# Kernel optimization log

Measured on AMD Instinct MI355X. Metric: run time of the kernel, lower is better.

The kernel has to match this reference:

```python
import jax, jax.numpy as jnp
import numpy as np

DIM, B, H, W = 96, 2, 64, 64
D_INNER, D_STATE, DT_RANK, K = 2 * DIM, 16, 6, 4


def _conv2d(x, w, b=None, padding=0, dilation=1, groups=1):
    out = jax.lax.conv_general_dilated(
        x, w, (1, 1), [(padding, padding)] * 2,
        rhs_dilation=(dilation, dilation),
        dimension_numbers=('NCHW', 'OIHW', 'NCHW'),
        feature_group_count=groups)
    return out if b is None else out + b[None, :, None, None]


def _layernorm(x, g, b, eps=1e-5):
    mu = x.mean(-1, keepdims=True)
    xc = x - mu
    var = (xc * xc).mean(-1, keepdims=True)
    return xc * jax.lax.rsqrt(var + eps) * g + b


def _chan_recal(t, w1, w2):
    s = t.mean((2, 3)) + t.max(axis=(2, 3))          # GAP + GMP, (B,C)
    w = jax.nn.sigmoid(jax.nn.relu(s @ w1.T) @ w2.T)
    return t * w[:, :, None, None]


def _selective_scan(u, delta, A, Bm, Cm, D):
    # u, delta: (B,K,d,L); A: (K,d,N); Bm,Cm: (B,K,N,L); D: (K,d)
    Bsz, Kk, d, L = u.shape
    N = A.shape[-1]
    seq = (jnp.moveaxis(delta, -1, 0), jnp.moveaxis(u, -1, 0),
           jnp.moveaxis(Bm, -1, 0), jnp.moveaxis(Cm, -1, 0))
    h0 = jnp.zeros((Bsz, Kk, d, N), u.dtype)

    def step(h, inp):
        dl, ul, bl, cl = inp  # (B,K,d),(B,K,d),(B,K,N),(B,K,N)
        h = jnp.exp(dl[..., None] * A) * h + (dl * ul)[..., None] * bl[:, :, None, :]
        return h, (h * cl[:, :, None, :]).sum(-1)

    _, ys = jax.lax.scan(step, h0, seq)
    return jnp.moveaxis(ys, 0, -1) + D[None, :, :, None] * u  # (B,K,d,L)


def _ss2d(x, in_proj_w, conv_w, conv_b, x_proj_w, dt_w, dt_b,
          A_logs, Ds, out_norm_g, out_norm_b, out_proj_w):
    Bsz, Hh, Ww, C = x.shape
    d = in_proj_w.shape[0] // 2
    xm, z = jnp.split(x @ in_proj_w.T, 2, axis=-1)
    xm = jnp.transpose(xm, (0, 3, 1, 2))  # (B,d,H,W)
    xm = jax.nn.silu(_conv2d(xm, conv_w, conv_b, padding=1, groups=d))
    L = Hh * Ww
    x_hw = xm.reshape(Bsz, d, L)
    x_wh = jnp.transpose(xm, (0, 1, 3, 2)).reshape(Bsz, d, L)
    xs = jnp.stack([x_hw, x_wh, x_hw[..., ::-1], x_wh[..., ::-1]], axis=1)  # (B,4,d,L)
    x_dbl = jnp.einsum('bkdl,kcd->bkcl', xs, x_proj_w)
    r = dt_w.shape[-1]
    N = A_logs.shape[-1]
    dts, Bs, Cs = jnp.split(x_dbl, [r, r + N], axis=2)
    dts = jax.nn.softplus(jnp.einsum('bkrl,kdr->bkdl', dts, dt_w) + dt_b[None, :, :, None])
    out_y = _selective_scan(xs, dts, -jnp.exp(A_logs), Bs, Cs, Ds)
    inv_y = out_y[:, 2:4, :, ::-1]
    wh = lambda t: jnp.transpose(t.reshape(Bsz, d, Ww, Hh), (0, 1, 3, 2)).reshape(Bsz, d, L)
    y = out_y[:, 0] + inv_y[:, 0] + wh(out_y[:, 1]) + wh(inv_y[:, 1])
    y = _layernorm(jnp.transpose(y, (0, 2, 1)).reshape(Bsz, Hh, Ww, d), out_norm_g, out_norm_b)
    return (y * jax.nn.silu(z)) @ out_proj_w.T


def _forward(x, arf_w1, arf_b1, arf_w2, arf_b2, arf_w3, arf_b3, arf_w4, arf_b4,
             fuse_w, fuse_b, edge_w, enh_w1, enh_b1, bn_g, bn_b, enh_w2, enh_b2,
             pre_fc1, pre_fc2, norm_g, norm_b, in_proj_w, ss_conv_w, ss_conv_b,
             x_proj_w, dt_w, dt_b, A_logs, Ds, out_norm_g, out_norm_b, out_proj_w,
             post_fc1, post_fc2, proj_w, proj_b):
    shortcut = x
    C = x.shape[1]
    g = C // 4
    # AdaptiveReceptiveField (fc gating branch is dead code in the original forward)
    f1 = _conv2d(x, arf_w1, arf_b1, padding=1, dilation=1, groups=g)
    f2 = _conv2d(x, arf_w2, arf_b2, padding=2, dilation=2, groups=g)
    f3 = _conv2d(x, arf_w3, arf_b3, padding=4, dilation=4, groups=g)
    f4 = _conv2d(x, arf_w4, arf_b4, padding=8, dilation=8, groups=g)
    h = _conv2d(jnp.concatenate([f1, f2, f3, f4], 1), fuse_w, fuse_b)
    # LearnableEdgeEnhancement (BatchNorm in training mode: batch stats, biased var)
    edge = _conv2d(h, edge_w, None, padding=1, groups=C)
    e = _conv2d(edge, enh_w1, enh_b1)
    mu = e.mean((0, 2, 3), keepdims=True)
    var = ((e - mu) ** 2).mean((0, 2, 3), keepdims=True)
    e = jax.nn.relu((e - mu) * jax.lax.rsqrt(var + 1e-5) * bn_g[None, :, None, None]
                    + bn_b[None, :, None, None])
    h = h * (1.0 + jax.nn.sigmoid(_conv2d(e, enh_w2, enh_b2)))
    h = _chan_recal(h, pre_fc1, pre_fc2)
    hn = _layernorm(jnp.transpose(h, (0, 2, 3, 1)), norm_g, norm_b)
    hn = _ss2d(hn, in_proj_w, ss_conv_w, ss_conv_b, x_proj_w, dt_w, dt_b,
               A_logs, Ds, out_norm_g, out_norm_b, out_proj_w)
    h = jnp.transpose(hn, (0, 3, 1, 2))
    h = _chan_recal(h, post_fc1, post_fc2)
    h = _conv2d(h, proj_w, proj_b)
    return shortcut + h


def setup_inputs():
    key = jax.random.key(0)
    ks = iter(jax.random.split(key, 48))
    rn = lambda shape, s=0.05: jax.random.normal(next(ks), shape, jnp.float32) * s
    lap = jnp.array([[0., 1., 0.], [1., -4., 1.], [0., 1., 0.]], jnp.float32)
    q = DIM // 4
    inp = {
        'x': jax.random.normal(next(ks), (B, DIM, H, W), jnp.float32),
        'arf_w1': rn((q, 4, 3, 3)), 'arf_b1': rn((q,)),
        'arf_w2': rn((q, 4, 3, 3)), 'arf_b2': rn((q,)),
        'arf_w3': rn((q, 4, 3, 3)), 'arf_b3': rn((q,)),
        'arf_w4': rn((q, 4, 3, 3)), 'arf_b4': rn((q,)),
        'fuse_w': rn((DIM, DIM, 1, 1)), 'fuse_b': rn((DIM,)),
        'edge_w': jnp.tile(lap[None, None], (DIM, 1, 1, 1)),
        'enh_w1': rn((q, DIM, 1, 1)), 'enh_b1': rn((q,)),
        'bn_g': jnp.ones((q,), jnp.float32), 'bn_b': jnp.zeros((q,), jnp.float32),
        'enh_w2': rn((DIM, q, 1, 1)), 'enh_b2': rn((DIM,)),
        'pre_fc1': rn((q, DIM)), 'pre_fc2': rn((DIM, q)),
        'norm_g': jnp.ones((DIM,), jnp.float32), 'norm_b': jnp.zeros((DIM,), jnp.float32),
        'in_proj_w': rn((2 * D_INNER, DIM)),
        'ss_conv_w': rn((D_INNER, 1, 3, 3)), 'ss_conv_b': rn((D_INNER,)),
        'x_proj_w': rn((K, DT_RANK + 2 * D_STATE, D_INNER)),
        'dt_w': rn((K, D_INNER, DT_RANK), 0.1), 'dt_b': rn((K, D_INNER), 0.1),
        'A_logs': jnp.broadcast_to(jnp.log(jnp.arange(1, D_STATE + 1, dtype=jnp.float32)),
                                   (K, D_INNER, D_STATE)) + jnp.zeros((K, D_INNER, D_STATE), jnp.float32),
        'Ds': jnp.ones((K, D_INNER), jnp.float32),
        'out_norm_g': jnp.ones((D_INNER,), jnp.float32),
        'out_norm_b': jnp.zeros((D_INNER,), jnp.float32),
        'out_proj_w': rn((DIM, D_INNER)),
        'post_fc1': rn((q, DIM)), 'post_fc2': rn((DIM, q)),
        'proj_w': rn((DIM, DIM, 1, 1)), 'proj_b': rn((DIM,)),
    }
    return inp


def reference(x, arf_w1, arf_b1, arf_w2, arf_b2, arf_w3, arf_b3, arf_w4, arf_b4,
              fuse_w, fuse_b, edge_w, enh_w1, enh_b1, bn_g, bn_b, enh_w2, enh_b2,
              pre_fc1, pre_fc2, norm_g, norm_b, in_proj_w, ss_conv_w, ss_conv_b,
              x_proj_w, dt_w, dt_b, A_logs, Ds, out_norm_g, out_norm_b, out_proj_w,
              post_fc1, post_fc2, proj_w, proj_b):
    return _forward(x, arf_w1, arf_b1, arf_w2, arf_b2, arf_w3, arf_b3, arf_w4, arf_b4,
                    fuse_w, fuse_b, edge_w, enh_w1, enh_b1, bn_g, bn_b, enh_w2, enh_b2,
                    pre_fc1, pre_fc2, norm_g, norm_b, in_proj_w, ss_conv_w, ss_conv_b,
                    x_proj_w, dt_w, dt_b, A_logs, Ds, out_norm_g, out_norm_b, out_proj_w,
                    post_fc1, post_fc2, proj_w, proj_b)
```

## Files before the change

kernel.cpp:

```cpp
#include <hip/hip_runtime.h>
#include <cmath>

#define LL   4096
#define HWD  64
#define CCH  96
#define QQ   24
#define DDI  192
#define NST  16
#define NCH  128
#define CLEN 32
#define TSC  32
#define XT2  32
#define XP   108

static const size_t OFF_F   = 0;
static const size_t OFF_H   = 786432;
static const size_t OFF_E   = 1572864;
static const size_t OFF_BN  = 1769472;
static const size_t OFF_S1  = 1769536;
static const size_t OFF_W1  = 1769728;
static const size_t OFF_S2  = 1769920;
static const size_t OFF_W2  = 1770112;
static const size_t OFF_HN  = 1770304;
static const size_t OFF_XM  = 2556736;
static const size_t OFF_Z   = 4129600;
static const size_t OFF_XC  = 5702464;
static const size_t OFF_DTS = 7275328;
static const size_t OFF_BC  = 13566784;
static const size_t OFF_YK  = 14615360;
static const size_t OFF_Y2  = 22528832;
static const size_t OFF_HL  = 23315264;
static const size_t OFF_SD  = 26460992;
static const size_t OFF_HIN = 26657600;

static __device__ __forceinline__ int map_k(int k, int l) {
  int ll = (k & 2) ? (LL - 1 - l) : l;
  return (k & 1) ? (((ll & 63) << 6) | (ll >> 6)) : ll;
}

__global__ __launch_bounds__(256) void k_arf(const float* __restrict__ x,
    const float* __restrict__ w1, const float* __restrict__ b1,
    const float* __restrict__ w2, const float* __restrict__ b2,
    const float* __restrict__ w3, const float* __restrict__ b3,
    const float* __restrict__ w4, const float* __restrict__ b4,
    float* __restrict__ f) {
  int idx = blockIdx.x * 256 + threadIdx.x;
  int p = idx & (LL - 1);
  int oc = __builtin_amdgcn_readfirstlane((idx >> 12) % CCH);
  int b  = __builtin_amdgcn_readfirstlane(idx / (CCH * LL));
  int i = oc / QQ, q = oc % QQ;
  int dil = 1 << i;
  const float* w  = (i == 0 ? w1 : i == 1 ? w2 : i == 2 ? w3 : w4) + q * 36;
  const float* bb = (i == 0 ? b1 : i == 1 ? b2 : i == 2 ? b3 : b4);
  int yy0 = p >> 6, xx0 = p & 63;
  float acc = bb[q];
  const float* xin = x + ((size_t)b * CCH + q * 4) * LL;
  #pragma unroll
  for (int ky = 0; ky < 3; ky++) {
    int yy = yy0 + (ky - 1) * dil;
    if (yy < 0 || yy >= HWD) continue;
    #pragma unroll
    for (int kx = 0; kx < 3; kx++) {
      int xx = xx0 + (kx - 1) * dil;
      if (xx < 0 || xx >= HWD) continue;
      int pp = (yy << 6) + xx;
      #pragma unroll
      for (int ci = 0; ci < 4; ci++)
        acc += w[ci * 9 + ky * 3 + kx] * xin[(size_t)ci * LL + pp];
    }
  }
  f[idx] = acc;
}

__global__ __launch_bounds__(256) void k_fuse(const float* __restrict__ f,
    const float* __restrict__ fw, const float* __restrict__ fb, float* __restrict__ h) {
  int idx = blockIdx.x * 256 + threadIdx.x;
  int p = idx & (LL - 1);
  int o = __builtin_amdgcn_readfirstlane((idx >> 12) % CCH);
  int b = __builtin_amdgcn_readfirstlane(idx / (CCH * LL));
  const float* fr = f + (size_t)b * CCH * LL + p;
  const float* wr = fw + o * CCH;
  float acc = fb[o];
  for (int c = 0; c < CCH; c++) acc += wr[c] * fr[(size_t)c * LL];
  h[idx] = acc;
}

__global__ __launch_bounds__(256) void k_edge(const float* __restrict__ h,
    const float* __restrict__ ew, float* __restrict__ edge) {
  int idx = blockIdx.x * 256 + threadIdx.x;
  int p = idx & (LL - 1);
  int c = __builtin_amdgcn_readfirstlane((idx >> 12) % CCH);
  int b = __builtin_amdgcn_readfirstlane(idx / (CCH * LL));
  int yy0 = p >> 6, xx0 = p & 63;
  const float* w = ew + c * 9;
  const float* hr = h + ((size_t)b * CCH + c) * LL;
  float acc = 0.f;
  #pragma unroll
  for (int ky = 0; ky < 3; ky++) {
    int yy = yy0 + ky - 1;
    if (yy < 0 || yy >= HWD) continue;
    #pragma unroll
    for (int kx = 0; kx < 3; kx++) {
      int xx = xx0 + kx - 1;
      if (xx < 0 || xx >= HWD) continue;
      acc += w[ky * 3 + kx] * hr[(yy << 6) + xx];
    }
  }
  edge[idx] = acc;
}

__global__ __launch_bounds__(256) void k_e1(const float* __restrict__ edge,
    const float* __restrict__ w, const float* __restrict__ bias, float* __restrict__ e) {
  int idx = blockIdx.x * 256 + threadIdx.x;
  int p = idx & (LL - 1);
  int q = __builtin_amdgcn_readfirstlane((idx >> 12) % QQ);
  int b = __builtin_amdgcn_readfirstlane(idx / (QQ * LL));
  const float* er = edge + (size_t)b * CCH * LL + p;
  const float* wr = w + q * CCH;
  float acc = bias[q];
  for (int c = 0; c < CCH; c++) acc += wr[c] * er[(size_t)c * LL];
  e[idx] = acc;
}

__global__ __launch_bounds__(256) void k_bnstats(const float* __restrict__ e,
    const float* __restrict__ g, const float* __restrict__ bb, float* __restrict__ bn) {
  int q = blockIdx.x, tid = threadIdx.x;
  __shared__ float rs[256], r2[256];
  float s = 0.f, s2 = 0.f;
  for (int b = 0; b < 2; b++) {
    const float* er = e + ((size_t)b * QQ + q) * LL;
    for (int p = tid; p < LL; p += 256) { float v = er[p]; s += v; s2 += v * v; }
  }
  rs[tid] = s; r2[tid] = s2; __syncthreads();
  for (int st = 128; st > 0; st >>= 1) {
    if (tid < st) { rs[tid] += rs[tid + st]; r2[tid] += r2[tid + st]; }
    __syncthreads();
  }
  if (tid == 0) {
    float mu = rs[0] / (2.f * LL);
    float var = r2[0] / (2.f * LL) - mu * mu;
    float sc = g[q] * rsqrtf(var + 1e-5f);
    bn[q] = sc;
    bn[QQ + q] = bb[q] - mu * sc;
  }
}

__global__ __launch_bounds__(256) void k_enh(const float* __restrict__ e,
    const float* __restrict__ bn, const float* __restrict__ w2,
    const float* __restrict__ b2, float* __restrict__ h) {
  int idx = blockIdx.x * 256 + threadIdx.x;
  int p = idx & (LL - 1);
  int o = __builtin_amdgcn_readfirstlane((idx >> 12) % CCH);
  int b = __builtin_amdgcn_readfirstlane(idx / (CCH * LL));
  const float* er = e + (size_t)b * QQ * LL + p;
  const float* wr = w2 + o * QQ;
  float acc = b2[o];
  #pragma unroll
  for (int q = 0; q < QQ; q++) {
    float en = fmaxf(er[(size_t)q * LL] * bn[q] + bn[QQ + q], 0.f);
    acc += wr[q] * en;
  }
  float sig = 1.f / (1.f + __expf(-acc));
  h[idx] *= (1.f + sig);
}

__global__ __launch_bounds__(256) void k_rowreduce(const float* __restrict__ t, float* __restrict__ sout) {
  int row = blockIdx.x, tid = threadIdx.x;
  __shared__ float rs[256], rm[256];
  float s = 0.f, m = -3.402823466e38f;
  const float* tr = t + (size_t)row * LL;
  for (int p = tid; p < LL; p += 256) { float v = tr[p]; s += v; m = fmaxf(m, v); }
  rs[tid] = s; rm[tid] = m; __syncthreads();
  for (int st = 128; st > 0; st >>= 1) {
    if (tid < st) { rs[tid] += rs[tid + st]; rm[tid] = fmaxf(rm[tid], rm[tid + st]); }
    __syncthreads();
  }
  if (tid == 0) sout[row] = rs[0] / (float)LL + rm[0];
}

__global__ __launch_bounds__(128) void k_recal_fc(const float* __restrict__ s1,
    const float* __restrict__ fc1, const float* __restrict__ fc2, float* __restrict__ wout) {
  int b = blockIdx.x, tid = threadIdx.x;
  __shared__ float sv[CCH];
  __shared__ float hid[QQ];
  if (tid < CCH) sv[tid] = s1[b * CCH + tid];
  __syncthreads();
  if (tid < QQ) {
    float a = 0.f;
    for (int c = 0; c < CCH; c++) a += sv[c] * fc1[tid * CCH + c];
    hid[tid] = fmaxf(a, 0.f);
  }
  __syncthreads();
  if (tid < CCH) {
    float a = 0.f;
    #pragma unroll
    for (int q = 0; q < QQ; q++) a += hid[q] * fc2[tid * QQ + q];
    wout[b * CCH + tid] = 1.f / (1.f + __expf(-a));
  }
}

__global__ __launch_bounds__(128) void k_recal_ln(const float* __restrict__ h,
    const float* __restrict__ w1buf, const float* __restrict__ ng,
    const float* __restrict__ nb, float* __restrict__ hn) {
  int pb = blockIdx.x;
  int b = pb >> 12, p = pb & (LL - 1);
  int tid = threadIdx.x;
  __shared__ float red[128];
  __shared__ float smu, srs;
  float v = 0.f;
  if (tid < CCH) v = h[((size_t)b * CCH + tid) * LL + p] * w1buf[b * CCH + tid];
  red[tid] = v; __syncthreads();
  for (int s = 64; s > 0; s >>= 1) { if (tid < s) red[tid] += red[tid + s]; __syncthreads(); }
  if (tid == 0) smu = red[0] / (float)CCH;
  __syncthreads();
  float xcv = (tid < CCH) ? v - smu : 0.f;
  red[tid] = xcv * xcv; __syncthreads();
  for (int s = 64; s > 0; s >>= 1) { if (tid < s) red[tid] += red[tid + s]; __syncthreads(); }
  if (tid == 0) srs = rsqrtf(red[0] / (float)CCH + 1e-5f);
  __syncthreads();
  if (tid < CCH) hn[((size_t)b * LL + p) * CCH + tid] = xcv * srs * ng[tid] + nb[tid];
}

__global__ __launch_bounds__(256) void k_inproj(const float* __restrict__ hn,
    const float* __restrict__ W, float* __restrict__ xm, float* __restrict__ z) {
  int pix0 = blockIdx.x * 64;
  int oc0 = blockIdx.y * CCH;
  int t = threadIdx.x;
  __shared__ float xs[64][XP];
  __shared__ float wbuf[CCH * CCH];
  for (int i = t; i < 64 * 24; i += 256) {
    int row = i / 24, dq = i % 24;
    *(float4*)(&xs[row][dq * 4]) = *(const float4*)(hn + (size_t)(pix0 + row) * CCH + dq * 4);
  }
  {
    const float4* src = (const float4*)(W + (size_t)oc0 * CCH);
    float4* dst = (float4*)wbuf;
    for (int i = t; i < CCH * 24; i += 256) dst[i] = src[i];
  }
  __syncthreads();
  int li = t & 63;
  int cg = __builtin_amdgcn_readfirstlane(t >> 6);
  float acc[24];
  #pragma unroll
  for (int j = 0; j < 24; j++) acc[j] = 0.f;
  for (int dq = 0; dq < 24; dq++) {
    float4 xv = *(const float4*)(&xs[li][dq * 4]);
    #pragma unroll
    for (int j = 0; j < 24; j++) {
      float4 wv = *(const float4*)(&wbuf[(cg + 4 * j) * CCH + dq * 4]);
      acc[j] = fmaf(xv.x, wv.x, fmaf(xv.y, wv.y, fmaf(xv.z, wv.z, fmaf(xv.w, wv.w, acc[j]))));
    }
  }
  __syncthreads();
  float* ot = &xs[0][0];
  #pragma unroll
  for (int j = 0; j < 24; j++) ot[li * 97 + cg + 4 * j] = acc[j];
  __syncthreads();
  float* dst = (oc0 < DDI) ? xm : z;
  int od0 = oc0 % DDI;
  for (int i = t; i < 64 * 96; i += 256) {
    int row = i / 96, c = i % 96;
    dst[(size_t)(pix0 + row) * DDI + od0 + c] = ot[row * 97 + c];
  }
}

__global__ __launch_bounds__(256) void k_ssconv(const float* __restrict__ xm,
    const float* __restrict__ w, const float* __restrict__ bias, float* __restrict__ xc) {
  int idx = blockIdx.x * 256 + threadIdx.x;
  int d = idx % DDI;
  int p = (idx / DDI) & (LL - 1);
  int b = idx / (DDI * LL);
  int yy0 = p >> 6, xx0 = p & 63;
  float acc = bias[d];
  const float* wr = w + d * 9;
  const float* xr = xm + (size_t)b * LL * DDI + d;
  #pragma unroll
  for (int ky = 0; ky < 3; ky++) {
    int yy = yy0 + ky - 1;
    if (yy < 0 || yy >= HWD) continue;
    #pragma unroll
    for (int kx = 0; kx < 3; kx++) {
      int xx = xx0 + kx - 1;
      if (xx < 0 || xx >= HWD) continue;
      acc += wr[ky * 3 + kx] * xr[(size_t)((yy << 6) + xx) * DDI];
    }
  }
  xc[(size_t)idx] = acc / (1.f + __expf(-acc));
}

__global__ __launch_bounds__(256) void k_xdbl(const float* __restrict__ xc,
    const float* __restrict__ xpw, float* __restrict__ dtr_ws, float* __restrict__ bcb) {
  int lt = blockIdx.x;
  int bk = blockIdx.y;
  int b = bk >> 2, k = bk & 3;
  int t = threadIdx.x;
  __shared__ float xs[XT2][XP];
  __shared__ float wbuf[38 * 96];
  int l0 = lt * XT2;
  int pos = t & 31;
  int cg = t >> 5;
  float acc[5];
  #pragma unroll
  for (int j = 0; j < 5; j++) acc[j] = 0.f;
  for (int h = 0; h < 2; h++) {
    __syncthreads();
    for (int i = t; i < XT2 * 24; i += 256) {
      int row = i / 24, dq = i % 24;
      int p = map_k(k, l0 + row);
      *(float4*)(&xs[row][dq * 4]) =
          *(const float4*)(xc + ((size_t)b * LL + p) * DDI + h * 96 + dq * 4);
    }
    for (int i = t; i < 38 * 24; i += 256) {
      int c = i / 24, dq = i % 24;
      *(float4*)(&wbuf[c * 96 + dq * 4]) =
          *(const float4*)(xpw + ((size_t)k * 38 + c) * DDI + h * 96 + dq * 4);
    }
    __syncthreads();
    for (int dq = 0; dq < 24; dq++) {
      float4 xv = *(const float4*)(&xs[pos][dq * 4]);
      #pragma unroll
      for (int j = 0; j < 5; j++) {
        int c = cg + 8 * j;
        if (c < 38) {
          float4 wv = *(const float4*)(&wbuf[c * 96 + dq * 4]);
          acc[j] = fmaf(xv.x, wv.x, fmaf(xv.y, wv.y, fmaf(xv.z, wv.z, fmaf(xv.w, wv.w, acc[j]))));
        }
      }
    }
  }
  #pragma unroll
  for (int j = 0; j < 5; j++) {
    int c = cg + 8 * j;
    if (c < 6) dtr_ws[((size_t)bk * LL + l0 + pos) * 6 + c] = acc[j];
    else if (c < 38) bcb[((size_t)bk * LL + l0 + pos) * 32 + (c - 6)] = acc[j];
  }
}

template <int PASS>
__global__ __launch_bounds__(192) void k_scan(const float* __restrict__ dtr_ws,
    const float* __restrict__ bcb, const float* __restrict__ xc,
    const float* __restrict__ A_logs, const float* __restrict__ dtw,
    const float* __restrict__ dtb, float* __restrict__ hl, float* __restrict__ sd,
    const float* __restrict__ hin, float* __restrict__ yk) {
  int ch = blockIdx.x, bk = blockIdx.y;
  int b = bk >> 2, k = bk & 3;
  int d = threadIdx.x;
  __shared__ float u_s[TSC][DDI];
  __shared__ float bcs[TSC][32];
  __shared__ float dtr_s[TSC][6];
  float Av[NST];
  #pragma unroll
  for (int n = 0; n < NST; n++) Av[n] = -__expf(A_logs[(size_t)(k * DDI + d) * NST + n]);
  bool pw = true;
  #pragma unroll
  for (int n = 1; n < NST; n++) pw = pw && (fabsf(Av[n] - (float)(n + 1) * Av[0]) <= 1e-3f * (n + 1));
  float wdt[6];
  #pragma unroll
  for (int r = 0; r < 6; r++) wdt[r] = dtw[((size_t)(k * DDI + d)) * 6 + r];
  float bdt = dtb[k * DDI + d];
  float h[NST];
  if (PASS == 0) {
    #pragma unroll
    for (int n = 0; n < NST; n++) h[n] = 0.f;
  } else {
    const float* hp = hin + ((size_t)(bk * DDI + d) * NCH + ch) * NST;
    #pragma unroll
    for (int n = 0; n < NST; n++) h[n] = hp[n];
  }
  float sumdt = 0.f;
  int l0 = ch * CLEN;
  {
    for (int i = d; i < TSC * (DDI / 4); i += 192) {
      int row = i / (DDI / 4), q = i % (DDI / 4);
      int p = map_k(k, l0 + row);
      ((float4*)u_s)[i] = *(const float4*)(xc + ((size_t)b * LL + p) * DDI + q * 4);
    }
    {
      const float4* src = (const float4*)(bcb + ((size_t)bk * LL + l0) * 32);
      float4* dst = (float4*)bcs;
      for (int i = d; i < TSC * 32 / 4; i += 192) dst[i] = src[i];
    }
    for (int i = d; i < TSC * 6; i += 192)
      ((float*)dtr_s)[i] = dtr_ws[((size_t)bk * LL + l0) * 6 + i];
    __syncthreads();
    for (int tt = 0; tt < TSC; tt++) {
      float a = bdt;
      #pragma unroll
      for (int r = 0; r < 6; r++) a = fmaf(wdt[r], dtr_s[tt][r], a);
      float dt = (a > 15.f) ? a : __logf(1.f + __expf(a));
      float u  = u_s[tt][d];
      float dtu = dt * u;
      if (PASS == 0) sumdt += dt;
      float eA[NST];
      if (pw) {
        float E = __expf(dt * Av[0]);
        float en = 1.f;
        #pragma unroll
        for (int n = 0; n < NST; n++) { en *= E; eA[n] = en; }
      } else {
        #pragma unroll
        for (int n = 0; n < NST; n++) eA[n] = __expf(dt * Av[n]);
      }
      float y = 0.f;
      #pragma unroll
      for (int n = 0; n < NST; n++) {
        h[n] = eA[n] * h[n] + dtu * bcs[tt][n];
        y += h[n] * bcs[tt][16 + n];
      }
      if (PASS == 1) {
        int p = map_k(k, l0 + tt);
        yk[((size_t)bk * LL + p) * DDI + d] = y;
      }
    }
  }
  if (PASS == 0) {
    float* hp = hl + ((size_t)(bk * DDI + d) * NCH + ch) * NST;
    #pragma unroll
    for (int n = 0; n < NST; n++) hp[n] = h[n];
    sd[(size_t)(bk * DDI + d) * NCH + ch] = sumdt;
  }
}

__global__ __launch_bounds__(256) void k_carry(const float* __restrict__ A_logs,
    const float* __restrict__ hl, const float* __restrict__ sd, float* __restrict__ hin) {
  int idx = blockIdx.x * 256 + threadIdx.x;
  int n = idx & 15;
  int d = (idx >> 4) % DDI;
  int bk = idx / (DDI * NST);
  int k = bk & 3;
  float Aval = -__expf(A_logs[(size_t)(k * DDI + d) * NST + n]);
  float h = 0.f;
  size_t base = (size_t)(bk * DDI + d) * NCH;
  for (int ch = 0; ch < NCH; ch++) {
    hin[(base + ch) * NST + n] = h;
    h = __expf(Aval * sd[base + ch]) * h + hl[(base + ch) * NST + n];
  }
}

__global__ __launch_bounds__(192) void k_combine(const float* __restrict__ yk,
    const float* __restrict__ xc, const float* __restrict__ Ds, const float* __restrict__ z,
    const float* __restrict__ ong, const float* __restrict__ onb, float* __restrict__ g) {
  int pb = blockIdx.x;
  int b = pb >> 12, p = pb & (LL - 1);
  int d = threadIdx.x;
  __shared__ float red[DDI];
  __shared__ float smu, srs;
  size_t base = ((size_t)b * 4 * LL + p) * DDI + d;
  float v = yk[base] + yk[base + (size_t)LL * DDI] + yk[base + 2ul * LL * DDI] + yk[base + 3ul * LL * DDI];
  v += (Ds[d] + Ds[DDI + d] + Ds[2 * DDI + d] + Ds[3 * DDI + d]) * xc[((size_t)b * LL + p) * DDI + d];
  red[d] = v; __syncthreads();
  if (d < 64) red[d] += red[d + 128];
  __syncthreads();
  for (int s = 64; s > 0; s >>= 1) { if (d < s) red[d] += red[d + s]; __syncthreads(); }
  if (d == 0) smu = red[0] / (float)DDI;
  __syncthreads();
  float xcv = v - smu;
  red[d] = xcv * xcv; __syncthreads();
  if (d < 64) red[d] += red[d + 128];
  __syncthreads();
  for (int s = 64; s > 0; s >>= 1) { if (d < s) red[d] += red[d + s]; __syncthreads(); }
  if (d == 0) srs = rsqrtf(red[0] / (float)DDI + 1e-5f);
  __syncthreads();
  float yv = xcv * srs * ong[d] + onb[d];
  float zz = z[((size_t)b * LL + p) * DDI + d];
  g[((size_t)b * LL + p) * DDI + d] = yv * (zz / (1.f + __expf(-zz)));
}

__global__ __launch_bounds__(256) void k_outproj(const float* __restrict__ g,
    const float* __restrict__ W, float* __restrict__ y2) {
  int pix0 = blockIdx.x * 64;
  int oc0 = blockIdx.y * 48;
  int b = pix0 >> 12, p0 = pix0 & (LL - 1);
  int t = threadIdx.x;
  __shared__ float xs[64][XP];
  __shared__ float wbuf[48 * 96];
  int li = t & 63;
  int cg = __builtin_amdgcn_readfirstlane(t >> 6);
  float acc[12];
  #pragma unroll
  for (int j = 0; j < 12; j++) acc[j] = 0.f;
  for (int h = 0; h < 2; h++) {
    __syncthreads();
    for (int i = t; i < 64 * 24; i += 256) {
      int row = i / 24, dq = i % 24;
      *(float4*)(&xs[row][dq * 4]) =
          *(const float4*)(g + (size_t)(pix0 + row) * DDI + h * 96 + dq * 4);
    }
    for (int i = t; i < 48 * 24; i += 256) {
      int c = i / 24, dq = i % 24;
      *(float4*)(&wbuf[c * 96 + dq * 4]) =
          *(const float4*)(W + (size_t)(oc0 + c) * DDI + h * 96 + dq * 4);
    }
    __syncthreads();
    for (int dq = 0; dq < 24; dq++) {
      float4 xv = *(const float4*)(&xs[li][dq * 4]);
      #pragma unroll
      for (int j = 0; j < 12; j++) {
        float4 wv = *(const float4*)(&wbuf[(cg + 4 * j) * 96 + dq * 4]);
        acc[j] = fmaf(xv.x, wv.x, fmaf(xv.y, wv.y, fmaf(xv.z, wv.z, fmaf(xv.w, wv.w, acc[j]))));
      }
    }
  }
  __syncthreads();
  float* ot = &xs[0][0];
  #pragma unroll
  for (int j = 0; j < 12; j++) ot[li * 49 + cg + 4 * j] = acc[j];
  __syncthreads();
  for (int i = t; i < 48 * 64; i += 256) {
    int o = i / 64, pi = i % 64;
    y2[((size_t)b * CCH + oc0 + o) * LL + p0 + pi] = ot[pi * 49 + o];
  }
}

__global__ __launch_bounds__(256) void k_final(const float* __restrict__ x,
    const float* __restrict__ y2, const float* __restrict__ w2buf,
    const float* __restrict__ pw, const float* __restrict__ pb, float* __restrict__ out) {
  int idx = blockIdx.x * 256 + threadIdx.x;
  int p = idx & (LL - 1);
  int c = __builtin_amdgcn_readfirstlane((idx >> 12) % CCH);
  int b = __builtin_amdgcn_readfirstlane(idx / (CCH * LL));
  const float* yr = y2 + (size_t)b * CCH * LL + p;
  const float* wr = pw + c * CCH;
  const float* wc = w2buf + b * CCH;
  float acc = pb[c];
  for (int o = 0; o < CCH; o++) acc += wr[o] * yr[(size_t)o * LL] * wc[o];
  out[idx] = x[idx] + acc;
}

extern "C" void kernel_launch(void* const* d_in, const int* in_sizes, int n_in,
                              void* d_out, int out_size, void* d_ws, size_t ws_size,
                              hipStream_t stream) {
  const float* x        = (const float*)d_in[0];
  const float* arf_w1   = (const float*)d_in[1];
  const float* arf_b1   = (const float*)d_in[2];
  const float* arf_w2   = (const float*)d_in[3];
  const float* arf_b2   = (const float*)d_in[4];
  const float* arf_w3   = (const float*)d_in[5];
  const float* arf_b3   = (const float*)d_in[6];
  const float* arf_w4   = (const float*)d_in[7];
  const float* arf_b4   = (const float*)d_in[8];
  const float* fuse_w   = (const float*)d_in[9];
  const float* fuse_b   = (const float*)d_in[10];
  const float* edge_w   = (const float*)d_in[11];
  const float* enh_w1   = (const float*)d_in[12];
  const float* enh_b1   = (const float*)d_in[13];
  const float* bn_g     = (const float*)d_in[14];
  const float* bn_b     = (const float*)d_in[15];
  const float* enh_w2   = (const float*)d_in[16];
  const float* enh_b2   = (const float*)d_in[17];
  const float* pre_fc1  = (const float*)d_in[18];
  const float* pre_fc2  = (const float*)d_in[19];
  const float* norm_g   = (const float*)d_in[20];
  const float* norm_b   = (const float*)d_in[21];
  const float* in_proj_w= (const float*)d_in[22];
  const float* ss_conv_w= (const float*)d_in[23];
  const float* ss_conv_b= (const float*)d_in[24];
  const float* x_proj_w = (const float*)d_in[25];
  const float* dt_w     = (const float*)d_in[26];
  const float* dt_b     = (const float*)d_in[27];
  const float* A_logs   = (const float*)d_in[28];
  const float* Ds       = (const float*)d_in[29];
  const float* out_ng   = (const float*)d_in[30];
  const float* out_nb   = (const float*)d_in[31];
  const float* out_proj_w = (const float*)d_in[32];
  const float* post_fc1 = (const float*)d_in[33];
  const float* post_fc2 = (const float*)d_in[34];
  const float* proj_w   = (const float*)d_in[35];
  const float* proj_b   = (const float*)d_in[36];

  float* ws = (float*)d_ws;
  float* fbuf  = ws + OFF_F;
  float* hbuf  = ws + OFF_H;
  float* ebuf  = ws + OFF_E;
  float* bnbuf = ws + OFF_BN;
  float* s1buf = ws + OFF_S1;
  float* w1buf = ws + OFF_W1;
  float* s2buf = ws + OFF_S2;
  float* w2buf = ws + OFF_W2;
  float* hnbuf = ws + OFF_HN;
  float* xmbuf = ws + OFF_XM;
  float* zbuf  = ws + OFF_Z;
  float* xcbuf = ws + OFF_XC;
  float* dtrbuf= ws + OFF_DTS;
  float* bcbuf = ws + OFF_BC;
  float* ykbuf = ws + OFF_YK;
  float* hlbuf = ws + OFF_HL;
  float* sdbuf = ws + OFF_SD;
  float* hinbuf= ws + OFF_HIN;
  float* y2buf = ws + OFF_Y2;
  float* gbuf  = xmbuf;

  k_arf<<<3072, 256, 0, stream>>>(x, arf_w1, arf_b1, arf_w2, arf_b2, arf_w3, arf_b3, arf_w4, arf_b4, fbuf);
  k_fuse<<<3072, 256, 0, stream>>>(fbuf, fuse_w, fuse_b, hbuf);
  k_edge<<<3072, 256, 0, stream>>>(hbuf, edge_w, fbuf);
  k_e1<<<768, 256, 0, stream>>>(fbuf, enh_w1, enh_b1, ebuf);
  k_bnstats<<<24, 256, 0, stream>>>(ebuf, bn_g, bn_b, bnbuf);
  k_enh<<<3072, 256, 0, stream>>>(ebuf, bnbuf, enh_w2, enh_b2, hbuf);
  k_rowreduce<<<192, 256, 0, stream>>>(hbuf, s1buf);
  k_recal_fc<<<2, 128, 0, stream>>>(s1buf, pre_fc1, pre_fc2, w1buf);
  k_recal_ln<<<8192, 128, 0, stream>>>(hbuf, w1buf, norm_g, norm_b, hnbuf);
  k_inproj<<<dim3(128, 4), 256, 0, stream>>>(hnbuf, in_proj_w, xmbuf, zbuf);
  k_ssconv<<<6144, 256, 0, stream>>>(xmbuf, ss_conv_w, ss_conv_b, xcbuf);
  k_xdbl<<<dim3(LL / XT2, 8), 256, 0, stream>>>(xcbuf, x_proj_w, dtrbuf, bcbuf);
  k_scan<0><<<dim3(NCH, 8), 192, 0, stream>>>(dtrbuf, bcbuf, xcbuf, A_logs, dt_w, dt_b, hlbuf, sdbuf, nullptr, nullptr);
  k_carry<<<96, 256, 0, stream>>>(A_logs, hlbuf, sdbuf, hinbuf);
  k_scan<1><<<dim3(NCH, 8), 192, 0, stream>>>(dtrbuf, bcbuf, xcbuf, A_logs, dt_w, dt_b, nullptr, nullptr, hinbuf, ykbuf);
  k_combine<<<8192, 192, 0, stream>>>(ykbuf, xcbuf, Ds, zbuf, out_ng, out_nb, gbuf);
  k_outproj<<<dim3(128, 2), 256, 0, stream>>>(gbuf, out_proj_w, y2buf);
  k_rowreduce<<<192, 256, 0, stream>>>(y2buf, s2buf);
  k_recal_fc<<<2, 128, 0, stream>>>(s2buf, post_fc1, post_fc2, w2buf);
  k_final<<<3072, 256, 0, stream>>>(x, y2buf, w2buf, proj_w, proj_b, (float*)d_out);
  (void)in_sizes; (void)n_in; (void)out_size; (void)ws_size;
}
```

Before: 246.5 us.

## Tile 1x1 convs via LDS, wave-shuffle layernorms, two-row depthwise conv

k_fuse and k_final become shared-memory tiled GEMMs over 64 pixels × 48 output channels with register accumulation, replacing the one-thread-per-output channel loop. k_final folds the recalibration weights into the staged weight tile. Both layernorm kernels (recal_ln, combine) now use one wavefront per pixel with shuffle reductions instead of LDS tree reductions with many barriers. The SS depthwise conv computes two vertically adjacent outputs per thread so the two rows can share loaded inputs. In exchange, launch grids shrink to 256 blocks for the GEMMs, which may underfill the GPU.

```diff
diff --git a/kernel.cpp b/kernel.cpp
--- a/kernel.cpp
+++ b/kernel.cpp
@@ -12,6 +12,7 @@
 #define TSC  32
 #define XT2  32
 #define XP   108
+#define FP   100
 
 static const size_t OFF_F   = 0;
 static const size_t OFF_H   = 786432;
@@ -74,15 +75,46 @@
 
 __global__ __launch_bounds__(256) void k_fuse(const float* __restrict__ f,
     const float* __restrict__ fw, const float* __restrict__ fb, float* __restrict__ h) {
-  int idx = blockIdx.x * 256 + threadIdx.x;
-  int p = idx & (LL - 1);
-  int o = __builtin_amdgcn_readfirstlane((idx >> 12) % CCH);
-  int b = __builtin_amdgcn_readfirstlane(idx / (CCH * LL));
-  const float* fr = f + (size_t)b * CCH * LL + p;
-  const float* wr = fw + o * CCH;
-  float acc = fb[o];
-  for (int c = 0; c < CCH; c++) acc += wr[c] * fr[(size_t)c * LL];
-  h[idx] = acc;
+  int pix0 = blockIdx.x * 64;
+  int oc0 = blockIdx.y * 48;
+  int b = pix0 >> 12, p0 = pix0 & (LL - 1);
+  int t = threadIdx.x;
+  __shared__ float fs[64][FP];
+  __shared__ float wbuf[48 * 96];
+  for (int i = t; i < 96 * 16; i += 256) {
+    int c = i >> 4, q = i & 15;
+    float4 v = *(const float4*)(f + ((size_t)b * CCH + c) * LL + p0 + q * 4);
+    fs[q * 4 + 0][c] = v.x; fs[q * 4 + 1][c] = v.y;
+    fs[q * 4 + 2][c] = v.z; fs[q * 4 + 3][c] = v.w;
+  }
+  {
+    const float4* src = (const float4*)(fw + (size_t)oc0 * CCH);
+    float4* dst = (float4*)wbuf;
+    for (int i = t; i < 48 * 24; i += 256) dst[i] = src[i];
+  }
+  __syncthreads();
+  int px = t & 63;
+  int cg = __builtin_amdgcn_readfirstlane(t >> 6);
+  float acc[12];
+  #pragma unroll
+  for (int j = 0; j < 12; j++) acc[j] = 0.f;
+  for (int c4 = 0; c4 < 24; c4++) {
+    float4 xv = *(const float4*)(&fs[px][c4 * 4]);
+    #pragma unroll
+    for (int j = 0; j < 12; j++) {
+      float4 wv = *(const float4*)(&wbuf[(cg * 12 + j) * 96 + c4 * 4]);
+      acc[j] = fmaf(xv.x, wv.x, fmaf(xv.y, wv.y, fmaf(xv.z, wv.z, fmaf(xv.w, wv.w, acc[j]))));
+    }
+  }
+  __syncthreads();
+  float* ot = &fs[0][0];
+  #pragma unroll
+  for (int j = 0; j < 12; j++) ot[px * 49 + cg * 12 + j] = acc[j];
+  __syncthreads();
+  for (int i = t; i < 48 * 64; i += 256) {
+    int o = i >> 6, p2 = i & 63;
+    h[((size_t)b * CCH + oc0 + o) * LL + p0 + p2] = ot[p2 * 49 + o] + fb[oc0 + o];
+  }
 }
 
 __global__ __launch_bounds__(256) void k_edge(const float* __restrict__ h,
@@ -199,26 +231,27 @@
   }
 }
 
-__global__ __launch_bounds__(128) void k_recal_ln(const float* __restrict__ h,
+__global__ __launch_bounds__(256) void k_recal_ln(const float* __restrict__ h,
     const float* __restrict__ w1buf, const float* __restrict__ ng,
     const float* __restrict__ nb, float* __restrict__ hn) {
-  int pb = blockIdx.x;
-  int b = pb >> 12, p = pb & (LL - 1);
-  int tid = threadIdx.x;
-  __shared__ float red[128];
-  __shared__ float smu, srs;
-  float v = 0.f;
-  if (tid < CCH) v = h[((size_t)b * CCH + tid) * LL + p] * w1buf[b * CCH + tid];
-  red[tid] = v; __syncthreads();
-  for (int s = 64; s > 0; s >>= 1) { if (tid < s) red[tid] += red[tid + s]; __syncthreads(); }
-  if (tid == 0) smu = red[0] / (float)CCH;
-  __syncthreads();
-  float xcv = (tid < CCH) ? v - smu : 0.f;
-  red[tid] = xcv * xcv; __syncthreads();
-  for (int s = 64; s > 0; s >>= 1) { if (tid < s) red[tid] += red[tid + s]; __syncthreads(); }
-  if (tid == 0) srs = rsqrtf(red[0] / (float)CCH + 1e-5f);
-  __syncthreads();
-  if (tid < CCH) hn[((size_t)b * LL + p) * CCH + tid] = xcv * srs * ng[tid] + nb[tid];
+  int pix = blockIdx.x * 4 + (threadIdx.x >> 6);
+  int b = pix >> 12, p = pix & (LL - 1);
+  int l = threadIdx.x & 63;
+  float v0 = h[((size_t)b * CCH + l) * LL + p] * w1buf[b * CCH + l];
+  float v1 = 0.f;
+  if (l < 32) v1 = h[((size_t)b * CCH + 64 + l) * LL + p] * w1buf[b * CCH + 64 + l];
+  float s = v0 + v1;
+  #pragma unroll
+  for (int o = 32; o > 0; o >>= 1) s += __shfl_xor(s, o);
+  float mu = s / (float)CCH;
+  float q = (v0 - mu) * (v0 - mu);
+  if (l < 32) q += (v1 - mu) * (v1 - mu);
+  #pragma unroll
+  for (int o = 32; o > 0; o >>= 1) q += __shfl_xor(q, o);
+  float rs = rsqrtf(q / (float)CCH + 1e-5f);
+  float* dst = hn + ((size_t)b * LL + p) * CCH;
+  dst[l] = (v0 - mu) * rs * ng[l] + nb[l];
+  if (l < 32) dst[64 + l] = (v1 - mu) * rs * ng[64 + l] + nb[64 + l];
 }
 
 __global__ __launch_bounds__(256) void k_inproj(const float* __restrict__ hn,
@@ -268,24 +301,31 @@
     const float* __restrict__ w, const float* __restrict__ bias, float* __restrict__ xc) {
   int idx = blockIdx.x * 256 + threadIdx.x;
   int d = idx % DDI;
-  int p = (idx / DDI) & (LL - 1);
-  int b = idx / (DDI * LL);
-  int yy0 = p >> 6, xx0 = p & 63;
-  float acc = bias[d];
-  const float* wr = w + d * 9;
+  int rem = idx / DDI;
+  int xx0 = rem & 63;
+  int y0 = ((rem >> 6) & 31) * 2;
+  int b = idx / (DDI * LL / 2);
+  float wv[9];
+  #pragma unroll
+  for (int i = 0; i < 9; i++) wv[i] = w[d * 9 + i];
+  float acc0 = bias[d], acc1 = bias[d];
   const float* xr = xm + (size_t)b * LL * DDI + d;
   #pragma unroll
-  for (int ky = 0; ky < 3; ky++) {
-    int yy = yy0 + ky - 1;
+  for (int ky = -1; ky <= 2; ky++) {
+    int yy = y0 + ky;
     if (yy < 0 || yy >= HWD) continue;
     #pragma unroll
-    for (int kx = 0; kx < 3; kx++) {
-      int xx = xx0 + kx - 1;
+    for (int kx = -1; kx <= 1; kx++) {
+      int xx = xx0 + kx;
       if (xx < 0 || xx >= HWD) continue;
-      acc += wr[ky * 3 + kx] * xr[(size_t)((yy << 6) + xx) * DDI];
-    }
-  }
-  xc[(size_t)idx] = acc / (1.f + __expf(-acc));
+      float val = xr[(size_t)((yy << 6) + xx) * DDI];
+      if (ky <= 1) acc0 += wv[(ky + 1) * 3 + (kx + 1)] * val;
+      if (ky >= 0) acc1 += wv[ky * 3 + (kx + 1)] * val;
+    }
+  }
+  size_t o0 = ((size_t)b * LL + (y0 << 6) + xx0) * DDI + d;
+  xc[o0] = acc0 / (1.f + __expf(-acc0));
+  xc[o0 + 64 * DDI] = acc1 / (1.f + __expf(-acc1));
 }
 
 __global__ __launch_bounds__(256) void k_xdbl(const float* __restrict__ xc,
@@ -437,33 +477,38 @@
   }
 }
 
-__global__ __launch_bounds__(192) void k_combine(const float* __restrict__ yk,
+__global__ __launch_bounds__(256) void k_combine(const float* __restrict__ yk,
     const float* __restrict__ xc, const float* __restrict__ Ds, const float* __restrict__ z,
     const float* __restrict__ ong, const float* __restrict__ onb, float* __restrict__ g) {
-  int pb = blockIdx.x;
-  int b = pb >> 12, p = pb & (LL - 1);
-  int d = threadIdx.x;
-  __shared__ float red[DDI];
-  __shared__ float smu, srs;
-  size_t base = ((size_t)b * 4 * LL + p) * DDI + d;
-  float v = yk[base] + yk[base + (size_t)LL * DDI] + yk[base + 2ul * LL * DDI] + yk[base + 3ul * LL * DDI];
-  v += (Ds[d] + Ds[DDI + d] + Ds[2 * DDI + d] + Ds[3 * DDI + d]) * xc[((size_t)b * LL + p) * DDI + d];
-  red[d] = v; __syncthreads();
-  if (d < 64) red[d] += red[d + 128];
-  __syncthreads();
-  for (int s = 64; s > 0; s >>= 1) { if (d < s) red[d] += red[d + s]; __syncthreads(); }
-  if (d == 0) smu = red[0] / (float)DDI;
-  __syncthreads();
-  float xcv = v - smu;
-  red[d] = xcv * xcv; __syncthreads();
-  if (d < 64) red[d] += red[d + 128];
-  __syncthreads();
-  for (int s = 64; s > 0; s >>= 1) { if (d < s) red[d] += red[d + s]; __syncthreads(); }
-  if (d == 0) srs = rsqrtf(red[0] / (float)DDI + 1e-5f);
-  __syncthreads();
-  float yv = xcv * srs * ong[d] + onb[d];
-  float zz = z[((size_t)b * LL + p) * DDI + d];
-  g[((size_t)b * LL + p) * DDI + d] = yv * (zz / (1.f + __expf(-zz)));
+  int pix = blockIdx.x * 4 + (threadIdx.x >> 6);
+  int b = pix >> 12, p = pix & (LL - 1);
+  int l = threadIdx.x & 63;
+  float v[3];
+  #pragma unroll
+  for (int m = 0; m < 3; m++) {
+    int d = l + 64 * m;
+    size_t base = ((size_t)b * 4 * LL + p) * DDI + d;
+    float tv = yk[base] + yk[base + (size_t)LL * DDI] + yk[base + 2ul * LL * DDI] + yk[base + 3ul * LL * DDI];
+    tv += (Ds[d] + Ds[DDI + d] + Ds[2 * DDI + d] + Ds[3 * DDI + d]) * xc[((size_t)b * LL + p) * DDI + d];
+    v[m] = tv;
+  }
+  float s = v[0] + v[1] + v[2];
+  #pragma unroll
+  for (int o = 32; o > 0; o >>= 1) s += __shfl_xor(s, o);
+  float mu = s / (float)DDI;
+  float q = 0.f;
+  #pragma unroll
+  for (int m = 0; m < 3; m++) q += (v[m] - mu) * (v[m] - mu);
+  #pragma unroll
+  for (int o = 32; o > 0; o >>= 1) q += __shfl_xor(q, o);
+  float rs = rsqrtf(q / (float)DDI + 1e-5f);
+  #pragma unroll
+  for (int m = 0; m < 3; m++) {
+    int d = l + 64 * m;
+    float yv = (v[m] - mu) * rs * ong[d] + onb[d];
+    float zz = z[((size_t)b * LL + p) * DDI + d];
+    g[((size_t)b * LL + p) * DDI + d] = yv * (zz / (1.f + __expf(-zz)));
+  }
 }
 
 __global__ __launch_bounds__(256) void k_outproj(const float* __restrict__ g,
@@ -515,16 +560,48 @@
 __global__ __launch_bounds__(256) void k_final(const float* __restrict__ x,
     const float* __restrict__ y2, const float* __restrict__ w2buf,
     const float* __restrict__ pw, const float* __restrict__ pb, float* __restrict__ out) {
-  int idx = blockIdx.x * 256 + threadIdx.x;
-  int p = idx & (LL - 1);
-  int c = __builtin_amdgcn_readfirstlane((idx >> 12) % CCH);
-  int b = __builtin_amdgcn_readfirstlane(idx / (CCH * LL));
-  const float* yr = y2 + (size_t)b * CCH * LL + p;
-  const float* wr = pw + c * CCH;
-  const float* wc = w2buf + b * CCH;
-  float acc = pb[c];
-  for (int o = 0; o < CCH; o++) acc += wr[o] * yr[(size_t)o * LL] * wc[o];
-  out[idx] = x[idx] + acc;
+  int pix0 = blockIdx.x * 64;
+  int oc0 = blockIdx.y * 48;
+  int b = pix0 >> 12, p0 = pix0 & (LL - 1);
+  int t = threadIdx.x;
+  __shared__ float fs[64][FP];
+  __shared__ float wbuf[48 * 96];
+  for (int i = t; i < 96 * 16; i += 256) {
+    int c = i >> 4, q = i & 15;
+    float4 v = *(const float4*)(y2 + ((size_t)b * CCH + c) * LL + p0 + q * 4);
+    fs[q * 4 + 0][c] = v.x; fs[q * 4 + 1][c] = v.y;
+    fs[q * 4 + 2][c] = v.z; fs[q * 4 + 3][c] = v.w;
+  }
+  for (int i = t; i < 48 * 24; i += 256) {
+    int row = i / 24, q = i % 24;
+    float4 wv = *(const float4*)(pw + (size_t)(oc0 + row) * CCH + q * 4);
+    float4 cv = *(const float4*)(w2buf + b * CCH + q * 4);
+    ((float4*)wbuf)[i] = make_float4(wv.x * cv.x, wv.y * cv.y, wv.z * cv.z, wv.w * cv.w);
+  }
+  __syncthreads();
+  int px = t & 63;
+  int cg = __builtin_amdgcn_readfirstlane(t >> 6);
+  float acc[12];
+  #pragma unroll
+  for (int j = 0; j < 12; j++) acc[j] = 0.f;
+  for (int c4 = 0; c4 < 24; c4++) {
+    float4 xv = *(const float4*)(&fs[px][c4 * 4]);
+    #pragma unroll
+    for (int j = 0; j < 12; j++) {
+      float4 wv = *(const float4*)(&wbuf[(cg * 12 + j) * 96 + c4 * 4]);
+      acc[j] = fmaf(xv.x, wv.x, fmaf(xv.y, wv.y, fmaf(xv.z, wv.z, fmaf(xv.w, wv.w, acc[j]))));
+    }
+  }
+  __syncthreads();
+  float* ot = &fs[0][0];
+  #pragma unroll
+  for (int j = 0; j < 12; j++) ot[px * 49 + cg * 12 + j] = acc[j];
+  __syncthreads();
+  for (int i = t; i < 48 * 64; i += 256) {
+    int o = i >> 6, p2 = i & 63;
+    size_t oi = ((size_t)b * CCH + oc0 + o) * LL + p0 + p2;
+    out[oi] = x[oi] + pb[oc0 + o] + ot[p2 * 49 + o];
+  }
 }
 
 extern "C" void kernel_launch(void* const* d_in, const int* in_sizes, int n_in,
@@ -591,24 +668,24 @@
   float* gbuf  = xmbuf;
 
   k_arf<<<3072, 256, 0, stream>>>(x, arf_w1, arf_b1, arf_w2, arf_b2, arf_w3, arf_b3, arf_w4, arf_b4, fbuf);
-  k_fuse<<<3072, 256, 0, stream>>>(fbuf, fuse_w, fuse_b, hbuf);
+  k_fuse<<<dim3(128, 2), 256, 0, stream>>>(fbuf, fuse_w, fuse_b, hbuf);
   k_edge<<<3072, 256, 0, stream>>>(hbuf, edge_w, fbuf);
   k_e1<<<768, 256, 0, stream>>>(fbuf, enh_w1, enh_b1, ebuf);
   k_bnstats<<<24, 256, 0, stream>>>(ebuf, bn_g, bn_b, bnbuf);
   k_enh<<<3072, 256, 0, stream>>>(ebuf, bnbuf, enh_w2, enh_b2, hbuf);
   k_rowreduce<<<192, 256, 0, stream>>>(hbuf, s1buf);
   k_recal_fc<<<2, 128, 0, stream>>>(s1buf, pre_fc1, pre_fc2, w1buf);
-  k_recal_ln<<<8192, 128, 0, stream>>>(hbuf, w1buf, norm_g, norm_b, hnbuf);
+  k_recal_ln<<<2048, 256, 0, stream>>>(hbuf, w1buf, norm_g, norm_b, hnbuf);
   k_inproj<<<dim3(128, 4), 256, 0, stream>>>(hnbuf, in_proj_w, xmbuf, zbuf);
-  k_ssconv<<<6144, 256, 0, stream>>>(xmbuf, ss_conv_w, ss_conv_b, xcbuf);
+  k_ssconv<<<3072, 256, 0, stream>>>(xmbuf, ss_conv_w, ss_conv_b, xcbuf);
   k_xdbl<<<dim3(LL / XT2, 8), 256, 0, stream>>>(xcbuf, x_proj_w, dtrbuf, bcbuf);
   k_scan<0><<<dim3(NCH, 8), 192, 0, stream>>>(dtrbuf, bcbuf, xcbuf, A_logs, dt_w, dt_b, hlbuf, sdbuf, nullptr, nullptr);
   k_carry<<<96, 256, 0, stream>>>(A_logs, hlbuf, sdbuf, hinbuf);
   k_scan<1><<<dim3(NCH, 8), 192, 0, stream>>>(dtrbuf, bcbuf, xcbuf, A_logs, dt_w, dt_b, nullptr, nullptr, hinbuf, ykbuf);
-  k_combine<<<8192, 192, 0, stream>>>(ykbuf, xcbuf, Ds, zbuf, out_ng, out_nb, gbuf);
+  k_combine<<<2048, 256, 0, stream>>>(ykbuf, xcbuf, Ds, zbuf, out_ng, out_nb, gbuf);
   k_outproj<<<dim3(128, 2), 256, 0, stream>>>(gbuf, out_proj_w, y2buf);
   k_rowreduce<<<192, 256, 0, stream>>>(y2buf, s2buf);
   k_recal_fc<<<2, 128, 0, stream>>>(s2buf, post_fc1, post_fc2, w2buf);
-  k_final<<<3072, 256, 0, stream>>>(x, y2buf, w2buf, proj_w, proj_b, (float*)d_out);
+  k_final<<<dim3(128, 2), 256, 0, stream>>>(x, y2buf, w2buf, proj_w, proj_b, (float*)d_out);
   (void)in_sizes; (void)n_in; (void)out_size; (void)ws_size;
 }
```

Measured after the change: 241.7 us. Within noise of the previous version (-1.9%).
